# Kernel tuning notes

Measured on AMD Instinct MI355X. Metric: run time of the kernel, lower is better.

## Reference

```python
import jax, jax.numpy as jnp
import numpy as np

B, C, O, H, W = 8, 256, 256, 64, 64
K = 3  # kernel size


def setup_inputs() -> dict:
    key = jax.random.key(0)
    k1, k2, k3 = jax.random.split(key, 3)
    x = jax.random.normal(k1, (B, C, H, W), dtype=jnp.float32)
    # offset-predicting conv: 18 = 2*K*K output channels (dy,dx per kernel tap).
    # Zero-init in the module; use small random weights so offsets are nontrivial.
    w_off = jax.random.normal(k2, (2 * K * K, C, K, K), dtype=jnp.float32) * 0.01
    b_off = jnp.zeros((2 * K * K,), dtype=jnp.float32)
    # deform conv weight, xavier-uniform (mmcv DeformConv has no bias)
    bound = float(np.sqrt(6.0 / (C * K * K + O * K * K)))
    w_def = jax.random.uniform(k3, (O, C, K, K), dtype=jnp.float32, minval=-bound, maxval=bound)
    return {"x": x, "w_off": w_off, "b_off": b_off, "w_def": w_def}


def _bilinear_gather(x, py, px):
    # x: [B,C,H,W]; py,px: [B,K2,Ho,Wo] float sample coords (zero padding outside)
    # returns [B,C,K2*Ho*Wo]
    Bb, Cc, Hh, Ww = x.shape
    y0f = jnp.floor(py); x0f = jnp.floor(px)
    wy = (py - y0f).reshape(Bb, 1, -1)
    wx = (px - x0f).reshape(Bb, 1, -1)
    y0 = y0f.astype(jnp.int32); x0 = x0f.astype(jnp.int32)
    flat = x.reshape(Bb, Cc, Hh * Ww)

    def gather(yi, xi):
        valid = ((yi >= 0) & (yi < Hh) & (xi >= 0) & (xi < Ww))
        yc = jnp.clip(yi, 0, Hh - 1); xc = jnp.clip(xi, 0, Ww - 1)
        idx = (yc * Ww + xc).reshape(Bb, 1, -1)
        g = jnp.take_along_axis(flat, jnp.broadcast_to(idx, (Bb, Cc, idx.shape[-1])), axis=2)
        return g * valid.reshape(Bb, 1, -1).astype(x.dtype)

    v00 = gather(y0, x0)
    v01 = gather(y0, x0 + 1)
    v10 = gather(y0 + 1, x0)
    v11 = gather(y0 + 1, x0 + 1)
    return (v00 * (1 - wy) * (1 - wx) + v01 * (1 - wy) * wx
            + v10 * wy * (1 - wx) + v11 * wy * wx)


def reference(x, w_off, b_off, w_def):
    # act -> offset conv -> deformable conv (norm = Identity)
    x = jax.nn.relu(x)
    offset = jax.lax.conv_general_dilated(
        x, w_off, (1, 1), ((1, 1), (1, 1)),
        dimension_numbers=('NCHW', 'OIHW', 'NCHW')) + b_off[None, :, None, None]
    Bb, Cc, Hh, Ww = x.shape
    Ho, Wo = offset.shape[2], offset.shape[3]
    K2 = K * K
    # mmcv offset layout: [B, 2*K2, H, W] with (dy, dx) pairs per kernel tap (row-major taps)
    off = offset.reshape(Bb, K2, 2, Ho, Wo)
    ky, kx = jnp.meshgrid(jnp.arange(K), jnp.arange(K), indexing='ij')
    ky = ky.reshape(-1).astype(x.dtype); kx = kx.reshape(-1).astype(x.dtype)
    # base sample positions: out_pos*stride - pad + tap  (stride=1, pad=1)
    base_y = jnp.arange(Ho, dtype=x.dtype)[None, :, None] - 1.0 + ky[:, None, None]  # [K2,Ho,1]
    base_x = jnp.arange(Wo, dtype=x.dtype)[None, None, :] - 1.0 + kx[:, None, None]  # [K2,1,Wo]
    py = base_y + off[:, :, 0]  # [B,K2,Ho,Wo]
    px = base_x + off[:, :, 1]
    samp = _bilinear_gather(x, py, px).reshape(Bb, Cc, K2, Ho, Wo)
    out = jnp.einsum('bckhw,ock->bohw', samp, w_def.reshape(w_def.shape[0], Cc, K2))
    return out
```

## Files before the change

kernel.cpp:

```cpp
#include <hip/hip_runtime.h>
#include <stdint.h>

#define B_ 8
#define C_ 256
#define O_ 256
#define HW_ 4096
#define RS 2560

typedef _Float16 f16x8 __attribute__((ext_vector_type(8)));
typedef __attribute__((ext_vector_type(4))) float f32x4;

__global__ __launch_bounds__(256) void k_nhwc2(const float* __restrict__ x,
                                               _Float16* __restrict__ xT) {
    int bh = blockIdx.x;
    int b = bh & 7, h = bh >> 3;
    int tid = threadIdx.x;
    __shared__ __align__(16) _Float16 s_t[64 * 72];
    int px = tid & 63, wg = tid >> 6;
    int px3 = tid >> 3, o8 = tid & 7;
#pragma unroll
    for (int half = 0; half < 4; ++half) {
        int c0 = half * 64;
        f16x8 va, vb;
#pragma unroll
        for (int j = 0; j < 8; ++j) {
            float f0 = x[((size_t)(b * C_ + c0 + wg * 16 + j)) * HW_ + h * 64 + px];
            float f1 = x[((size_t)(b * C_ + c0 + wg * 16 + 8 + j)) * HW_ + h * 64 + px];
            va[j] = (_Float16)fmaxf(f0, 0.f);
            vb[j] = (_Float16)fmaxf(f1, 0.f);
        }
        if (half) __syncthreads();
        *reinterpret_cast<f16x8*>(&s_t[px * 72 + wg * 16]) = va;
        *reinterpret_cast<f16x8*>(&s_t[px * 72 + wg * 16 + 8]) = vb;
        __syncthreads();
#pragma unroll
        for (int it = 0; it < 2; ++it) {
            int p = it * 32 + px3;
            f16x8 w = *reinterpret_cast<const f16x8*>(&s_t[p * 72 + o8 * 8]);
            *reinterpret_cast<f16x8*>(
                &xT[((size_t)((b * 64 + h) * 64 + p)) * C_ + c0 + o8 * 8]) = w;
        }
    }
}

__global__ void k_prep_wdef(const float* __restrict__ w_def, _Float16* __restrict__ wfrag) {
    int idx = blockIdx.x * 256 + threadIdx.x;
    if (idx >= 9 * 8 * 16 * 64) return;
    int lane = idx & 63;
    int mfg = (idx >> 6) & 15;
    int ccc = (idx >> 10) & 7;
    int k2 = idx >> 13;
    int o = mfg * 16 + (lane & 15);
    int cb = ccc * 32 + (lane >> 4) * 8;
    f16x8 pk;
#pragma unroll
    for (int j = 0; j < 8; ++j)
        pk[j] = (_Float16)w_def[(size_t)(o * C_ + cb + j) * 9 + k2];
    *reinterpret_cast<f16x8*>(wfrag + (size_t)idx * 8) = pk;
}

__global__ void k_prep_woffrag(const float* __restrict__ w_off, _Float16* __restrict__ wfr) {
    int idx = blockIdx.x * 256 + threadIdx.x;
    if (idx >= 9 * 8 * 2 * 64) return;
    int lane = idx & 63;
    int mfg = (idx >> 6) & 1;
    int ccc = (idx >> 7) & 7;
    int k2 = idx >> 10;
    int o = mfg * 16 + (lane & 15);
    int cb = ccc * 32 + (lane >> 4) * 8;
    f16x8 pk;
#pragma unroll
    for (int j = 0; j < 8; ++j)
        pk[j] = (o < 18) ? (_Float16)w_off[(size_t)(o * C_ + cb + j) * 9 + k2] : (_Float16)0.f;
    *reinterpret_cast<f16x8*>(wfr + (size_t)idx * 8) = pk;
}

__global__ __launch_bounds__(256) void k_offconv4(const _Float16* __restrict__ xT,
                                                  const _Float16* __restrict__ wofr,
                                                  const float* __restrict__ b_off,
                                                  float* __restrict__ offs) {
    int bh = blockIdx.x;
    int b = bh & 7, h = bh >> 3;
    int tid = threadIdx.x, lane = tid & 63, wm = tid >> 6;
    int px = wm * 16 + (lane & 15);
    int chl = (lane >> 4) * 8;
    f32x4 acc0 = (f32x4){0.f, 0.f, 0.f, 0.f};
    f32x4 acc1 = (f32x4){0.f, 0.f, 0.f, 0.f};
    const _Float16* xb = xT + (size_t)b * HW_ * C_;
    for (int k2 = 0; k2 < 9; ++k2) {
        int y = h + k2 / 3 - 1;
        int xs = px + k2 % 3 - 1;
        bool v = ((unsigned)y < 64u) && ((unsigned)xs < 64u);
        int yc = y < 0 ? 0 : (y > 63 ? 63 : y);
        int xc = xs < 0 ? 0 : (xs > 63 ? 63 : xs);
        const _Float16* xp = xb + (size_t)(yc * 64 + xc) * C_ + chl;
#pragma unroll
        for (int q = 0; q < 8; ++q) {
            f16x8 bf = *reinterpret_cast<const f16x8*>(xp + q * 32);
            if (!v) bf = (f16x8)(_Float16)0.f;
            const f16x8* wp = reinterpret_cast<const f16x8*>(wofr) +
                              (size_t)((k2 * 8 + q) * 2) * 64 + lane;
            acc0 = __builtin_amdgcn_mfma_f32_16x16x32_f16(wp[0], bf, acc0, 0, 0, 0);
            acc1 = __builtin_amdgcn_mfma_f32_16x16x32_f16(wp[64], bf, acc1, 0, 0, 0);
        }
    }
#pragma unroll
    for (int r = 0; r < 4; ++r) {
        int oc = (lane >> 4) * 4 + r;
        offs[(((size_t)b * 18 + oc) * 64 + h) * 64 + px] = acc0[r] + b_off[oc];
    }
#pragma unroll
    for (int r = 0; r < 4; ++r) {
        int oc = 16 + (lane >> 4) * 4 + r;
        if (oc < 18)
            offs[(((size_t)b * 18 + oc) * 64 + h) * 64 + px] = acc1[r] + b_off[oc];
    }
}

__global__ __launch_bounds__(256, 3) void k_deform12(const _Float16* __restrict__ xT,
                                                     const _Float16* __restrict__ wfrag,
                                                     const float* __restrict__ offs,
                                                     float* __restrict__ out) {
    int blk = blockIdx.x;
    int b = blk & 7, h = blk >> 3;
    int tid = threadIdx.x, lane = tid & 63, wm = tid >> 6;
    int gp = tid & 63, gq = tid >> 6;

    __shared__ uint4 s_geo[576];
    __shared__ __align__(16) _Float16 s_x[5 * RS];
    __shared__ __align__(16) _Float16 s_samp[2][64 * 40];

    const _Float16* xb = xT + (size_t)b * HW_ * C_;

    int spx = tid >> 2, so = tid & 3;
    f16x8 st[5];
#define STAGE_LOAD(CQ)                                                             \
    {                                                                              \
        _Pragma("unroll") for (int r = 0; r < 5; ++r)                              \
        {                                                                          \
            int yr = h - 2 + r;                                                    \
            yr = yr < 0 ? 0 : (yr > 63 ? 63 : yr);                                 \
            st[r] = *reinterpret_cast<const f16x8*>(                               \
                xb + (size_t)(yr * 64 + spx) * C_ + (CQ) * 32 + so * 8);           \
        }                                                                          \
    }
#define STAGE_WRITE()                                                              \
    {                                                                              \
        _Pragma("unroll") for (int r = 0; r < 5; ++r)                              \
            *reinterpret_cast<f16x8*>(&s_x[r * RS + spx * 40 + so * 8]) = st[r];   \
    }

    STAGE_LOAD(0);

    for (int idx = tid; idx < 576; idx += 256) {
        int k2 = idx >> 6, p = idx & 63;
        float dy = offs[(((size_t)b * 18 + k2 * 2 + 0) * 64 + h) * 64 + p];
        float dx = offs[(((size_t)b * 18 + k2 * 2 + 1) * 64 + h) * 64 + p];
        float py = (float)(h - 1 + k2 / 3) + dy;
        float pxx = (float)(p - 1 + k2 % 3) + dx;
        float y0f = floorf(py), x0f = floorf(pxx);
        float wy = py - y0f, wx = pxx - x0f;
        int y0 = (int)y0f, x0 = (int)x0f;
        float w00 = (1.f - wy) * (1.f - wx), w01 = (1.f - wy) * wx;
        float w10 = wy * (1.f - wx), w11 = wy * wx;
        bool vy0 = (unsigned)y0 < 64u, vy1 = (unsigned)(y0 + 1) < 64u;
        bool vx0 = (unsigned)x0 < 64u, vx1 = (unsigned)(x0 + 1) < 64u;
        if (!(vy0 && vx0)) w00 = 0.f;
        if (!(vy0 && vx1)) w01 = 0.f;
        if (!(vy1 && vx0)) w10 = 0.f;
        if (!(vy1 && vx1)) w11 = 0.f;
        union { _Float16 h2[2]; unsigned u; } p01, p23;
        p01.h2[0] = (_Float16)w00; p01.h2[1] = (_Float16)w01;
        p23.h2[0] = (_Float16)w10; p23.h2[1] = (_Float16)w11;
        int x0c = x0 < 0 ? 0 : (x0 > 63 ? 63 : x0);
        int x1c = (x0 + 1) < 0 ? 0 : ((x0 + 1) > 63 ? 63 : (x0 + 1));
        int y0c = y0 < 0 ? 0 : (y0 > 63 ? 63 : y0);
        int y1c = (y0 + 1) < 0 ? 0 : ((y0 + 1) > 63 ? 63 : (y0 + 1));
        int ry0 = y0 - (h - 2);
        unsigned flag = (ry0 >= 0 && ry0 <= 3) ? (unsigned)ry0 : 255u;
        uint4 g;
        g.x = p01.u;
        g.y = p23.u;
        g.z = (unsigned)x0c | ((unsigned)x1c << 16);
        g.w = (unsigned)y0c | ((unsigned)y1c << 8) | (flag << 16);
        s_geo[idx] = g;
    }

    STAGE_WRITE();
    asm volatile("s_waitcnt lgkmcnt(0)" ::: "memory");
    __builtin_amdgcn_s_barrier();

    f32x4 acc[4][4];
#pragma unroll
    for (int i = 0; i < 4; ++i)
#pragma unroll
        for (int j = 0; j < 4; ++j) acc[i][j] = (f32x4){0.f, 0.f, 0.f, 0.f};

#define LOADA(DST, T)                                                              \
    {                                                                              \
        const f16x8* wf = reinterpret_cast<const f16x8*>(wfrag) +                  \
                          ((size_t)(T) * 16 + wm * 4) * 64 + lane;                 \
        _Pragma("unroll") for (int mf = 0; mf < 4; ++mf) DST[mf] = wf[mf * 64];    \
    }

#define PACKSTEP(K2, BUF, CQ)                                                      \
    {                                                                              \
        uint4 gg = s_geo[(K2) * 64 + gp];                                          \
        union { unsigned u; _Float16 h2[2]; } p01, p23;                            \
        p01.u = gg.x; p23.u = gg.y;                                                \
        int x0c = gg.z & 0xFFFF, x1c = gg.z >> 16;                                 \
        int flag = gg.w >> 16;                                                     \
        f16x8 c00, c01, c10, c11;                                                  \
        if (flag <= 3) {                                                           \
            const _Float16* b0 = s_x + flag * RS + gq * 8;                         \
            c00 = *reinterpret_cast<const f16x8*>(b0 + x0c * 40);                  \
            c01 = *reinterpret_cast<const f16x8*>(b0 + x1c * 40);                  \
            c10 = *reinterpret_cast<const f16x8*>(b0 + RS + x0c * 40);             \
            c11 = *reinterpret_cast<const f16x8*>(b0 + RS + x1c * 40);             \
        } else {                                                                   \
            int y0c = gg.w & 0xFF, y1c = (gg.w >> 8) & 0xFF;                       \
            const _Float16* gb = xb + (CQ) * 32 + gq * 8;                          \
            c00 = *reinterpret_cast<const f16x8*>(gb + (size_t)(y0c * 64 + x0c) * C_); \
            c01 = *reinterpret_cast<const f16x8*>(gb + (size_t)(y0c * 64 + x1c) * C_); \
            c10 = *reinterpret_cast<const f16x8*>(gb + (size_t)(y1c * 64 + x0c) * C_); \
            c11 = *reinterpret_cast<const f16x8*>(gb + (size_t)(y1c * 64 + x1c) * C_); \
        }                                                                          \
        f16x8 pk = c00 * p01.h2[0] + c01 * p01.h2[1] + c10 * p23.h2[0] + c11 * p23.h2[1]; \
        *reinterpret_cast<f16x8*>(&s_samp[BUF][gp * 40 + gq * 8]) = pk;            \
    }

    f16x8 Ac[4], An[4];
    LOADA(Ac, 0);
#pragma unroll
    for (int mf = 0; mf < 4; ++mf) An[mf] = Ac[mf];

    for (int cq = 0; cq < 8; ++cq) {
        PACKSTEP(0, 0, cq);
        asm volatile("s_waitcnt lgkmcnt(0)" ::: "memory");
        __builtin_amdgcn_s_barrier();

        if (cq < 7) STAGE_LOAD(cq + 1);

#pragma unroll
        for (int k2 = 0; k2 < 9; ++k2) {
            if (k2 < 8) {
                LOADA(An, (k2 + 1) * 8 + cq);
            } else if (cq < 7) {
                LOADA(An, cq + 1);
            }

            f16x8 bfr[4];
#pragma unroll
            for (int nf = 0; nf < 4; ++nf) {
                int n = nf * 16 + (lane & 15);
                bfr[nf] = *reinterpret_cast<const f16x8*>(
                    &s_samp[k2 & 1][n * 40 + (lane >> 4) * 8]);
            }

#pragma unroll
            for (int mf = 0; mf < 4; ++mf)
#pragma unroll
                for (int nf = 0; nf < 4; ++nf)
                    acc[mf][nf] = __builtin_amdgcn_mfma_f32_16x16x32_f16(
                        Ac[mf], bfr[nf], acc[mf][nf], 0, 0, 0);

            if (k2 < 8) PACKSTEP(k2 + 1, (k2 + 1) & 1, cq);
#pragma unroll
            for (int mf = 0; mf < 4; ++mf) Ac[mf] = An[mf];

            asm volatile("s_waitcnt lgkmcnt(0)" ::: "memory");
            __builtin_amdgcn_s_barrier();
        }

        if (cq < 7) {
            STAGE_WRITE();
            asm volatile("s_waitcnt lgkmcnt(0)" ::: "memory");
            __builtin_amdgcn_s_barrier();
        }
    }

    float* op = out + (size_t)b * O_ * HW_ + h * 64;
#pragma unroll
    for (int mf = 0; mf < 4; ++mf)
#pragma unroll
        for (int nf = 0; nf < 4; ++nf)
#pragma unroll
            for (int r = 0; r < 4; ++r) {
                int o = wm * 64 + mf * 16 + (lane >> 4) * 4 + r;
                int w = nf * 16 + (lane & 15);
                op[(size_t)o * HW_ + w] = acc[mf][nf][r];
            }
}

extern "C" void kernel_launch(void* const* d_in, const int* in_sizes, int n_in,
                              void* d_out, int out_size, void* d_ws, size_t ws_size,
                              hipStream_t stream) {
    const float* x = (const float*)d_in[0];
    const float* w_off = (const float*)d_in[1];
    const float* b_off = (const float*)d_in[2];
    const float* w_def = (const float*)d_in[3];
    float* out = (float*)d_out;
    char* ws = (char*)d_ws;

    float* offs = (float*)ws;
    _Float16* xT = (_Float16*)(ws + 2359296);
    _Float16* wfrag = (_Float16*)(ws + 2359296 + 16777216);
    _Float16* wofr = (_Float16*)(ws + 2359296 + 16777216 + 1179648);

    k_nhwc2<<<512, 256, 0, stream>>>(x, xT);
    k_prep_wdef<<<288, 256, 0, stream>>>(w_def, wfrag);
    k_prep_woffrag<<<36, 256, 0, stream>>>(w_off, wofr);
    k_offconv4<<<512, 256, 0, stream>>>(xT, wofr, b_off, offs);
    k_deform12<<<512, 256, 0, stream>>>(xT, wfrag, offs, out);
}
```

Baseline: 107.0 us.

## Flatten deform conv loop into triple-buffered software pipeline with double-buffered x staging

```diff
diff --git a/kernel.cpp b/kernel.cpp
--- a/kernel.cpp
+++ b/kernel.cpp
@@ -117,7 +117,7 @@
     }
 }
 
-__global__ __launch_bounds__(256, 3) void k_deform12(const _Float16* __restrict__ xT,
+__global__ __launch_bounds__(256, 2) void k_deform13(const _Float16* __restrict__ xT,
                                                      const _Float16* __restrict__ wfrag,
                                                      const float* __restrict__ offs,
                                                      float* __restrict__ out) {
@@ -127,8 +127,8 @@
     int gp = tid & 63, gq = tid >> 6;
 
     __shared__ uint4 s_geo[576];
-    __shared__ __align__(16) _Float16 s_x[5 * RS];
-    __shared__ __align__(16) _Float16 s_samp[2][64 * 40];
+    __shared__ __align__(16) _Float16 s_x[2][5 * RS];
+    __shared__ __align__(16) _Float16 s_samp[3][64 * 40];
 
     const _Float16* xb = xT + (size_t)b * HW_ * C_;
 
@@ -144,10 +144,10 @@
                 xb + (size_t)(yr * 64 + spx) * C_ + (CQ) * 32 + so * 8);           \
         }                                                                          \
     }
-#define STAGE_WRITE()                                                              \
+#define STAGE_WRITE(PAR)                                                           \
     {                                                                              \
         _Pragma("unroll") for (int r = 0; r < 5; ++r)                              \
-            *reinterpret_cast<f16x8*>(&s_x[r * RS + spx * 40 + so * 8]) = st[r];   \
+            *reinterpret_cast<f16x8*>(&s_x[PAR][r * RS + spx * 40 + so * 8]) = st[r]; \
     }
 
     STAGE_LOAD(0);
@@ -186,7 +186,7 @@
         s_geo[idx] = g;
     }
 
-    STAGE_WRITE();
+    STAGE_WRITE(0);
     asm volatile("s_waitcnt lgkmcnt(0)" ::: "memory");
     __builtin_amdgcn_s_barrier();
 
@@ -203,23 +203,25 @@
         _Pragma("unroll") for (int mf = 0; mf < 4; ++mf) DST[mf] = wf[mf * 64];    \
     }
 
-#define PACKSTEP(K2, BUF, CQ)                                                      \
-    {                                                                              \
-        uint4 gg = s_geo[(K2) * 64 + gp];                                          \
+#define PACKSTEP(T, BUF)                                                           \
+    {                                                                              \
+        int t_ = (T);                                                              \
+        int cqt_ = t_ / 9, k2t_ = t_ - cqt_ * 9;                                   \
+        uint4 gg = s_geo[k2t_ * 64 + gp];                                          \
         union { unsigned u; _Float16 h2[2]; } p01, p23;                            \
         p01.u = gg.x; p23.u = gg.y;                                                \
         int x0c = gg.z & 0xFFFF, x1c = gg.z >> 16;                                 \
         int flag = gg.w >> 16;                                                     \
         f16x8 c00, c01, c10, c11;                                                  \
         if (flag <= 3) {                                                           \
-            const _Float16* b0 = s_x + flag * RS + gq * 8;                         \
+            const _Float16* b0 = &s_x[cqt_ & 1][flag * RS + gq * 8];               \
             c00 = *reinterpret_cast<const f16x8*>(b0 + x0c * 40);                  \
             c01 = *reinterpret_cast<const f16x8*>(b0 + x1c * 40);                  \
             c10 = *reinterpret_cast<const f16x8*>(b0 + RS + x0c * 40);             \
             c11 = *reinterpret_cast<const f16x8*>(b0 + RS + x1c * 40);             \
         } else {                                                                   \
             int y0c = gg.w & 0xFF, y1c = (gg.w >> 8) & 0xFF;                       \
-            const _Float16* gb = xb + (CQ) * 32 + gq * 8;                          \
+            const _Float16* gb = xb + cqt_ * 32 + gq * 8;                          \
             c00 = *reinterpret_cast<const f16x8*>(gb + (size_t)(y0c * 64 + x0c) * C_); \
             c01 = *reinterpret_cast<const f16x8*>(gb + (size_t)(y0c * 64 + x1c) * C_); \
             c10 = *reinterpret_cast<const f16x8*>(gb + (size_t)(y1c * 64 + x0c) * C_); \
@@ -230,54 +232,60 @@
     }
 
     f16x8 Ac[4], An[4];
+
+    PACKSTEP(0, 0);
+    PACKSTEP(1, 1);
     LOADA(Ac, 0);
 #pragma unroll
     for (int mf = 0; mf < 4; ++mf) An[mf] = Ac[mf];
-
-    for (int cq = 0; cq < 8; ++cq) {
-        PACKSTEP(0, 0, cq);
-        asm volatile("s_waitcnt lgkmcnt(0)" ::: "memory");
-        __builtin_amdgcn_s_barrier();
-
-        if (cq < 7) STAGE_LOAD(cq + 1);
-
-#pragma unroll
-        for (int k2 = 0; k2 < 9; ++k2) {
-            if (k2 < 8) {
-                LOADA(An, (k2 + 1) * 8 + cq);
-            } else if (cq < 7) {
-                LOADA(An, cq + 1);
-            }
-
-            f16x8 bfr[4];
-#pragma unroll
-            for (int nf = 0; nf < 4; ++nf) {
-                int n = nf * 16 + (lane & 15);
-                bfr[nf] = *reinterpret_cast<const f16x8*>(
-                    &s_samp[k2 & 1][n * 40 + (lane >> 4) * 8]);
-            }
-
-#pragma unroll
-            for (int mf = 0; mf < 4; ++mf)
-#pragma unroll
-                for (int nf = 0; nf < 4; ++nf)
-                    acc[mf][nf] = __builtin_amdgcn_mfma_f32_16x16x32_f16(
-                        Ac[mf], bfr[nf], acc[mf][nf], 0, 0, 0);
-
-            if (k2 < 8) PACKSTEP(k2 + 1, (k2 + 1) & 1, cq);
-#pragma unroll
-            for (int mf = 0; mf < 4; ++mf) Ac[mf] = An[mf];
-
-            asm volatile("s_waitcnt lgkmcnt(0)" ::: "memory");
-            __builtin_amdgcn_s_barrier();
-        }
-
-        if (cq < 7) {
-            STAGE_WRITE();
-            asm volatile("s_waitcnt lgkmcnt(0)" ::: "memory");
-            __builtin_amdgcn_s_barrier();
-        }
-    }
+    asm volatile("s_waitcnt lgkmcnt(0)" ::: "memory");
+    __builtin_amdgcn_s_barrier();
+
+#define STEP(S_, BUFJ, PBUF, LASTWAIT)                                             \
+    {                                                                              \
+        int s_ = (S_);                                                             \
+        int cq_ = s_ / 9, k2_ = s_ - cq_ * 9;                                      \
+        f16x8 bfr[4];                                                              \
+        _Pragma("unroll") for (int nf = 0; nf < 4; ++nf)                           \
+        {                                                                          \
+            int n = nf * 16 + (lane & 15);                                         \
+            bfr[nf] = *reinterpret_cast<const f16x8*>(                             \
+                &s_samp[BUFJ][n * 40 + (lane >> 4) * 8]);                          \
+        }                                                                          \
+        if (k2_ == 0 && cq_ < 7) STAGE_LOAD(cq_ + 1);                              \
+        if (k2_ == 4 && cq_ < 7) STAGE_WRITE((cq_ + 1) & 1);                       \
+        if (s_ + 2 < 72) PACKSTEP(s_ + 2, PBUF);                                   \
+        if (s_ + 1 < 72) {                                                         \
+            int s1 = s_ + 1;                                                       \
+            int c1 = s1 / 9;                                                       \
+            LOADA(An, (s1 - c1 * 9) * 8 + c1);                                     \
+        }                                                                          \
+        _Pragma("unroll") for (int mf = 0; mf < 4; ++mf)                           \
+            _Pragma("unroll") for (int nf = 0; nf < 4; ++nf)                       \
+                acc[mf][nf] = __builtin_amdgcn_mfma_f32_16x16x32_f16(              \
+                    Ac[mf], bfr[nf], acc[mf][nf], 0, 0, 0);                        \
+        if (s_ + 1 < 72) {                                                         \
+            _Pragma("unroll") for (int mf = 0; mf < 4; ++mf) Ac[mf] = An[mf];      \
+        }                                                                          \
+        if (LASTWAIT) {                                                            \
+            asm volatile("s_waitcnt lgkmcnt(0)" ::: "memory");                     \
+        } else {                                                                   \
+            asm volatile("s_waitcnt lgkmcnt(1)" ::: "memory");                     \
+        }                                                                          \
+        __builtin_amdgcn_s_barrier();                                              \
+        __builtin_amdgcn_sched_barrier(0);                                         \
+    }
+
+#pragma unroll 1
+    for (int ss = 0; ss < 23; ++ss) {
+        int s0 = ss * 3;
+        STEP(s0 + 0, 0, 2, 0);
+        STEP(s0 + 1, 1, 0, 0);
+        STEP(s0 + 2, 2, 1, 0);
+    }
+    STEP(69, 0, 2, 1);
+    STEP(70, 1, 0, 1);
+    STEP(71, 2, 1, 1);
 
     float* op = out + (size_t)b * O_ * HW_ + h * 64;
 #pragma unroll
@@ -311,5 +319,5 @@
     k_prep_wdef<<<288, 256, 0, stream>>>(w_def, wfrag);
     k_prep_woffrag<<<36, 256, 0, stream>>>(w_off, wofr);
     k_offconv4<<<512, 256, 0, stream>>>(xT, wofr, b_off, offs);
-    k_deform12<<<512, 256, 0, stream>>>(xT, wfrag, offs, out);
-}
+    k_deform13<<<512, 256, 0, stream>>>(xT, wfrag, offs, out);
+}
```

Result: slower. 116.1 us (+8.5%).

## Warp-specialize deform kernel into producer and MFMA consumer waves

Applied to the files above, without the earlier changes.

```diff
diff --git a/kernel.cpp b/kernel.cpp
--- a/kernel.cpp
+++ b/kernel.cpp
@@ -117,22 +117,22 @@
     }
 }
 
-__global__ __launch_bounds__(256, 3) void k_deform12(const _Float16* __restrict__ xT,
+__global__ __launch_bounds__(512, 4) void k_deform14(const _Float16* __restrict__ xT,
                                                      const _Float16* __restrict__ wfrag,
                                                      const float* __restrict__ offs,
                                                      float* __restrict__ out) {
     int blk = blockIdx.x;
     int b = blk & 7, h = blk >> 3;
-    int tid = threadIdx.x, lane = tid & 63, wm = tid >> 6;
-    int gp = tid & 63, gq = tid >> 6;
+    int tid = threadIdx.x, lane = tid & 63, wid = tid >> 6;
 
     __shared__ uint4 s_geo[576];
-    __shared__ __align__(16) _Float16 s_x[5 * RS];
-    __shared__ __align__(16) _Float16 s_samp[2][64 * 40];
+    __shared__ __align__(16) _Float16 s_x[2][5 * RS];
+    __shared__ __align__(16) _Float16 s_samp[3][64 * 40];
 
     const _Float16* xb = xT + (size_t)b * HW_ * C_;
 
-    int spx = tid >> 2, so = tid & 3;
+    int gp = tid & 63, gq = (tid >> 6) & 3;
+    int spx = (tid & 255) >> 2, so = tid & 3;
     f16x8 st[5];
 #define STAGE_LOAD(CQ)                                                             \
     {                                                                              \
@@ -144,15 +144,17 @@
                 xb + (size_t)(yr * 64 + spx) * C_ + (CQ) * 32 + so * 8);           \
         }                                                                          \
     }
-#define STAGE_WRITE()                                                              \
+#define STAGE_WRITE(PAR)                                                           \
     {                                                                              \
         _Pragma("unroll") for (int r = 0; r < 5; ++r)                              \
-            *reinterpret_cast<f16x8*>(&s_x[r * RS + spx * 40 + so * 8]) = st[r];   \
-    }
-
-    STAGE_LOAD(0);
-
-    for (int idx = tid; idx < 576; idx += 256) {
+            *reinterpret_cast<f16x8*>(&s_x[PAR][r * RS + spx * 40 + so * 8]) = st[r]; \
+    }
+
+    bool is_prod = (wid < 4);
+
+    if (is_prod) STAGE_LOAD(0);
+
+    for (int idx = tid; idx < 576; idx += 512) {
         int k2 = idx >> 6, p = idx & 63;
         float dy = offs[(((size_t)b * 18 + k2 * 2 + 0) * 64 + h) * 64 + p];
         float dx = offs[(((size_t)b * 18 + k2 * 2 + 1) * 64 + h) * 64 + p];
@@ -186,40 +188,29 @@
         s_geo[idx] = g;
     }
 
-    STAGE_WRITE();
+    if (is_prod) STAGE_WRITE(0);
     asm volatile("s_waitcnt lgkmcnt(0)" ::: "memory");
     __builtin_amdgcn_s_barrier();
 
-    f32x4 acc[4][4];
-#pragma unroll
-    for (int i = 0; i < 4; ++i)
-#pragma unroll
-        for (int j = 0; j < 4; ++j) acc[i][j] = (f32x4){0.f, 0.f, 0.f, 0.f};
-
-#define LOADA(DST, T)                                                              \
+#define PACKSTEP(T, BUF)                                                           \
     {                                                                              \
-        const f16x8* wf = reinterpret_cast<const f16x8*>(wfrag) +                  \
-                          ((size_t)(T) * 16 + wm * 4) * 64 + lane;                 \
-        _Pragma("unroll") for (int mf = 0; mf < 4; ++mf) DST[mf] = wf[mf * 64];    \
-    }
-
-#define PACKSTEP(K2, BUF, CQ)                                                      \
-    {                                                                              \
-        uint4 gg = s_geo[(K2) * 64 + gp];                                          \
+        int t_ = (T);                                                              \
+        int cqt_ = t_ / 9, k2t_ = t_ - cqt_ * 9;                                   \
+        uint4 gg = s_geo[k2t_ * 64 + gp];                                          \
         union { unsigned u; _Float16 h2[2]; } p01, p23;                            \
         p01.u = gg.x; p23.u = gg.y;                                                \
         int x0c = gg.z & 0xFFFF, x1c = gg.z >> 16;                                 \
         int flag = gg.w >> 16;                                                     \
         f16x8 c00, c01, c10, c11;                                                  \
         if (flag <= 3) {                                                           \
-            const _Float16* b0 = s_x + flag * RS + gq * 8;                         \
+            const _Float16* b0 = &s_x[cqt_ & 1][flag * RS + gq * 8];               \
             c00 = *reinterpret_cast<const f16x8*>(b0 + x0c * 40);                  \
             c01 = *reinterpret_cast<const f16x8*>(b0 + x1c * 40);                  \
             c10 = *reinterpret_cast<const f16x8*>(b0 + RS + x0c * 40);             \
             c11 = *reinterpret_cast<const f16x8*>(b0 + RS + x1c * 40);             \
         } else {                                                                   \
             int y0c = gg.w & 0xFF, y1c = (gg.w >> 8) & 0xFF;                       \
-            const _Float16* gb = xb + (CQ) * 32 + gq * 8;                          \
+            const _Float16* gb = xb + cqt_ * 32 + gq * 8;                          \
             c00 = *reinterpret_cast<const f16x8*>(gb + (size_t)(y0c * 64 + x0c) * C_); \
             c01 = *reinterpret_cast<const f16x8*>(gb + (size_t)(y0c * 64 + x1c) * C_); \
             c10 = *reinterpret_cast<const f16x8*>(gb + (size_t)(y1c * 64 + x0c) * C_); \
@@ -229,34 +220,48 @@
         *reinterpret_cast<f16x8*>(&s_samp[BUF][gp * 40 + gq * 8]) = pk;            \
     }
 
-    f16x8 Ac[4], An[4];
-    LOADA(Ac, 0);
-#pragma unroll
-    for (int mf = 0; mf < 4; ++mf) An[mf] = Ac[mf];
-
-    for (int cq = 0; cq < 8; ++cq) {
-        PACKSTEP(0, 0, cq);
+    if (is_prod) {
+        PACKSTEP(0, 0);
         asm volatile("s_waitcnt lgkmcnt(0)" ::: "memory");
         __builtin_amdgcn_s_barrier();
 
-        if (cq < 7) STAGE_LOAD(cq + 1);
-
-#pragma unroll
-        for (int k2 = 0; k2 < 9; ++k2) {
-            if (k2 < 8) {
-                LOADA(An, (k2 + 1) * 8 + cq);
-            } else if (cq < 7) {
-                LOADA(An, cq + 1);
-            }
-
+#pragma unroll 1
+        for (int t = 1; t < 72; ++t) {
+            int cqt = t / 9, k2t = t - cqt * 9;
+            if (k2t == 1 && cqt < 7) STAGE_LOAD(cqt + 1);
+            if (k2t == 7 && cqt < 7) STAGE_WRITE((cqt + 1) & 1);
+            PACKSTEP(t, t % 3);
+            asm volatile("s_waitcnt lgkmcnt(0)" ::: "memory");
+            __builtin_amdgcn_s_barrier();
+        }
+        __builtin_amdgcn_s_barrier();
+    } else {
+        int wc = wid - 4;
+        f32x4 acc[4][4];
+#pragma unroll
+        for (int i = 0; i < 4; ++i)
+#pragma unroll
+            for (int j = 0; j < 4; ++j) acc[i][j] = (f32x4){0.f, 0.f, 0.f, 0.f};
+
+        __builtin_amdgcn_s_barrier();
+        __builtin_amdgcn_sched_barrier(0);
+
+#pragma unroll 1
+        for (int s = 0; s < 72; ++s) {
+            int cq = s / 9, k2 = s - cq * 9;
+            f16x8 Ac[4];
+            const f16x8* wf = reinterpret_cast<const f16x8*>(wfrag) +
+                              ((size_t)((k2 * 8 + cq) * 16) + wc * 4) * 64 + lane;
+#pragma unroll
+            for (int mf = 0; mf < 4; ++mf) Ac[mf] = wf[(size_t)mf * 64];
+
+            const _Float16* sb = s_samp[s % 3];
             f16x8 bfr[4];
 #pragma unroll
             for (int nf = 0; nf < 4; ++nf) {
                 int n = nf * 16 + (lane & 15);
-                bfr[nf] = *reinterpret_cast<const f16x8*>(
-                    &s_samp[k2 & 1][n * 40 + (lane >> 4) * 8]);
+                bfr[nf] = *reinterpret_cast<const f16x8*>(&sb[n * 40 + (lane >> 4) * 8]);
             }
-
 #pragma unroll
             for (int mf = 0; mf < 4; ++mf)
 #pragma unroll
@@ -264,32 +269,22 @@
                     acc[mf][nf] = __builtin_amdgcn_mfma_f32_16x16x32_f16(
                         Ac[mf], bfr[nf], acc[mf][nf], 0, 0, 0);
 
-            if (k2 < 8) PACKSTEP(k2 + 1, (k2 + 1) & 1, cq);
-#pragma unroll
-            for (int mf = 0; mf < 4; ++mf) Ac[mf] = An[mf];
-
-            asm volatile("s_waitcnt lgkmcnt(0)" ::: "memory");
             __builtin_amdgcn_s_barrier();
-        }
-
-        if (cq < 7) {
-            STAGE_WRITE();
-            asm volatile("s_waitcnt lgkmcnt(0)" ::: "memory");
-            __builtin_amdgcn_s_barrier();
-        }
-    }
-
-    float* op = out + (size_t)b * O_ * HW_ + h * 64;
-#pragma unroll
-    for (int mf = 0; mf < 4; ++mf)
-#pragma unroll
-        for (int nf = 0; nf < 4; ++nf)
-#pragma unroll
-            for (int r = 0; r < 4; ++r) {
-                int o = wm * 64 + mf * 16 + (lane >> 4) * 4 + r;
-                int w = nf * 16 + (lane & 15);
-                op[(size_t)o * HW_ + w] = acc[mf][nf][r];
-            }
+            __builtin_amdgcn_sched_barrier(0);
+        }
+
+        float* op = out + (size_t)b * O_ * HW_ + h * 64;
+#pragma unroll
+        for (int mf = 0; mf < 4; ++mf)
+#pragma unroll
+            for (int nf = 0; nf < 4; ++nf)
+#pragma unroll
+                for (int r = 0; r < 4; ++r) {
+                    int o = wc * 64 + mf * 16 + (lane >> 4) * 4 + r;
+                    int w = nf * 16 + (lane & 15);
+                    op[(size_t)o * HW_ + w] = acc[mf][nf][r];
+                }
+    }
 }
 
 extern "C" void kernel_launch(void* const* d_in, const int* in_sizes, int n_in,
@@ -311,5 +306,5 @@
     k_prep_wdef<<<288, 256, 0, stream>>>(w_def, wfrag);
     k_prep_woffrag<<<36, 256, 0, stream>>>(w_off, wofr);
     k_offconv4<<<512, 256, 0, stream>>>(xT, wofr, b_off, offs);
-    k_deform12<<<512, 256, 0, stream>>>(xT, wfrag, offs, out);
-}
+    k_deform14<<<512, 512, 0, stream>>>(xT, wfrag, offs, out);
+}
```

New measurement: 106.4 us. About the same (-0.5%).
